# Performance work log

Hardware: AMD Instinct MI355X
Metric: run time of the kernel (lower is better)

## Reference

```python
import jax, jax.numpy as jnp
import numpy as np

B, S, HID = 2, 2048, 2048
NH, NKV, D = 32, 8, 64
M = 256          # FAVOR+ random features
CHUNK = 128      # causal chunk size
EPS = 1e-6


def setup_inputs():
    key = jax.random.key(0)
    ks = jax.random.split(key, 7)
    hidden_states = jax.random.normal(ks[0], (B, S, HID), jnp.float32)
    # RoPE tables (HF Llama style): [B, S, D]
    inv_freq = 1.0 / (10000.0 ** (jnp.arange(0, D, 2, dtype=jnp.float32) / D))
    freqs = jnp.arange(S, dtype=jnp.float32)[:, None] * inv_freq[None, :]   # [S, D/2]
    emb = jnp.concatenate([freqs, freqs], axis=-1)                          # [S, D]
    cos = jnp.broadcast_to(jnp.cos(emb)[None], (B, S, D)).astype(jnp.float32)
    sin = jnp.broadcast_to(jnp.sin(emb)[None], (B, S, D)).astype(jnp.float32)
    sc = 0.02
    Wq = jax.random.normal(ks[1], (NH * D, HID), jnp.float32) * sc
    Wk = jax.random.normal(ks[2], (NKV * D, HID), jnp.float32) * sc
    Wv = jax.random.normal(ks[3], (NKV * D, HID), jnp.float32) * sc
    Wo = jax.random.normal(ks[4], (HID, NH * D), jnp.float32) * sc
    proj = jax.random.normal(ks[5], (M, D), jnp.float32)  # FAVOR+ random projection
    return {"hidden_states": hidden_states, "cos": cos, "sin": sin,
            "Wq": Wq, "Wk": Wk, "Wv": Wv, "Wo": Wo, "proj": proj}


def rotate_half(x):
    x1, x2 = x[..., : x.shape[-1] // 2], x[..., x.shape[-1] // 2:]
    return jnp.concatenate([-x2, x1], axis=-1)


def favor_features(x, proj, is_query):
    # FAVOR+ positive softmax-kernel features: phi(x) = exp(Wx' - |x'|^2/2 - stab)/sqrt(m)
    dn = x.shape[-1] ** -0.25
    xn = x * dn                                            # data normalizer d^{-1/4}
    xp = jnp.einsum('bhsd,md->bhsm', xn, proj)             # [B,H,S,M]
    sq = 0.5 * jnp.sum(xn * xn, axis=-1, keepdims=True)
    if is_query:
        stab = jnp.max(xp, axis=-1, keepdims=True)
    else:
        stab = jnp.max(xp, axis=(-1, -2), keepdims=True)
    return (jnp.exp(xp - sq - stab) + EPS) / jnp.sqrt(jnp.asarray(M, xp.dtype))


def causal_linear_attention(phi_q, phi_k, v):
    # phi_q/phi_k: [B,H,S,M], v: [B,H,S,D]; causal chunked prefix formulation
    Bh, H, T, m = phi_q.shape
    d = v.shape[-1]
    nc = T // CHUNK
    qc = phi_q.reshape(Bh, H, nc, CHUNK, m)
    kc = phi_k.reshape(Bh, H, nc, CHUNK, m)
    vc = v.reshape(Bh, H, nc, CHUNK, d)
    # per-chunk KV state and key sums
    kv = jnp.einsum('bhscm,bhscd->bhsmd', kc, vc)          # [B,H,nc,M,D]
    kz = jnp.sum(kc, axis=3)                               # [B,H,nc,M]
    kv_pre = jnp.cumsum(kv, axis=2) - kv                   # exclusive prefix
    kz_pre = jnp.cumsum(kz, axis=2) - kz
    inter = jnp.einsum('bhscm,bhsmd->bhscd', qc, kv_pre)
    inter_z = jnp.einsum('bhscm,bhsm->bhsc', qc, kz_pre)
    # intra-chunk causal part
    mask = jnp.tril(jnp.ones((CHUNK, CHUNK), phi_q.dtype))
    scores = jnp.einsum('bhscm,bhstm->bhsct', qc, kc) * mask
    intra = jnp.einsum('bhsct,bhstd->bhscd', scores, vc)
    intra_z = jnp.sum(scores, axis=-1)
    out = (inter + intra) / (inter_z + intra_z + EPS)[..., None]
    return out.reshape(Bh, H, T, d)


def reference(hidden_states, cos, sin, Wq, Wk, Wv, Wo, proj):
    b, s, _ = hidden_states.shape
    q = (hidden_states @ Wq.T).reshape(b, s, NH, D).transpose(0, 2, 1, 3)   # [B,NH,S,D]
    k = (hidden_states @ Wk.T).reshape(b, s, NKV, D).transpose(0, 2, 1, 3)  # [B,NKV,S,D]
    v = (hidden_states @ Wv.T).reshape(b, s, NKV, D).transpose(0, 2, 1, 3)
    c, si = cos[:, None, :, :], sin[:, None, :, :]
    q = q * c + rotate_half(q) * si
    k = k * c + rotate_half(k) * si
    groups = NH // NKV
    k = jnp.repeat(k, groups, axis=1)
    v = jnp.repeat(v, groups, axis=1)
    phi_q = favor_features(q, proj, is_query=True)
    phi_k = favor_features(k, proj, is_query=False)
    attn = causal_linear_attention(phi_q, phi_k, v)                         # [B,NH,S,D]
    attn = attn.transpose(0, 2, 1, 3).reshape(b, s, NH * D)
    return attn @ Wo.T
```

## Files before the change

kernel.cpp:

```cpp
#include <hip/hip_runtime.h>
#include <hip/hip_bf16.h>

#define SEQ   2048
#define NHEAD 32
#define NKVH  8
#define DH    64
#define MFEAT 256
#define NCH   16
#define EPSF  1e-6f

typedef __hip_bfloat16 bf16;
typedef unsigned short u16;
typedef __attribute__((ext_vector_type(8))) short short8;
typedef __attribute__((ext_vector_type(4))) float f32x4;

__device__ __forceinline__ float b2f(bf16 x){ return __bfloat162float(x); }
__device__ __forceinline__ bf16  f2b(float x){ return __float2bfloat16(x); }
__device__ __forceinline__ u16   f2u(float x){ bf16 h = __float2bfloat16(x); return *reinterpret_cast<u16*>(&h); }

__device__ __forceinline__ bool probe_f32(const unsigned* __restrict__ p){
  return (p[0] & 0xFFFFu) == 0u;
}
__device__ __forceinline__ float loadIn(const void* __restrict__ ptr, size_t idx, bool f32){
  return f32 ? ((const float*)ptr)[idx] : b2f(((const bf16*)ptr)[idx]);
}

__device__ __forceinline__ void cp16(u16* lds, const u16* g){
  __builtin_amdgcn_global_load_lds((const __attribute__((address_space(1))) unsigned*)g,
      (__attribute__((address_space(3))) unsigned*)lds, 16, 0, 0);
}

#define MFMA16(a,b,c) __builtin_amdgcn_mfma_f32_16x16x32_bf16(a,b,c,0,0,0)

__global__ __launch_bounds__(256) void conv_kernel(const void* __restrict__ src,
    u16* __restrict__ dst, const unsigned* __restrict__ probe)
{
  const bool f32in = probe_f32(probe);
  size_t i = ((size_t)blockIdx.x*256 + threadIdx.x)*4;
  #pragma unroll
  for (int j=0;j<4;++j) dst[i+j] = f2u(loadIn(src, i+j, f32in));
}

__global__ __launch_bounds__(256) void gemm_mfma(const u16* __restrict__ A,
    const u16* __restrict__ W, float* __restrict__ oq, float* __restrict__ ok,
    float* __restrict__ ov, void* __restrict__ outAny, int K, int N, int mode,
    const void* __restrict__ cosg, const void* __restrict__ sing,
    const unsigned* __restrict__ probe)
{
  __shared__ __align__(16) u16 sA[4096];
  __shared__ __align__(16) u16 sB[4096];
  const int tid = threadIdx.x;
  const int lane = tid & 63, wave = tid >> 6;
  const int c0 = blockIdx.x*128, r0 = blockIdx.y*128;
  const int wm = wave & 1, wn = wave >> 1;
  f32x4 acc[4][4] = {};

  const int ch0 = wave*64 + lane, ch1 = 256 + wave*64 + lane;
  const u16* gA0 = A + (size_t)(r0 + (ch0>>2))*K + (ch0&3)*8;
  const u16* gA1 = A + (size_t)(r0 + (ch1>>2))*K + (ch1&3)*8;
  const u16* gB0 = W + (size_t)(c0 + (ch0>>2))*K + (ch0&3)*8;
  const u16* gB1 = W + (size_t)(c0 + (ch1>>2))*K + (ch1&3)*8;
  u16* lA0 = &sA[(wave*64)*8];  u16* lA1 = &sA[(256 + wave*64)*8];
  u16* lB0 = &sB[(wave*64)*8];  u16* lB1 = &sB[(256 + wave*64)*8];

  const u16* pA = &sA[(wm*64 + (lane&15))*32 + (lane>>4)*8];
  const u16* pB = &sB[(wn*64 + (lane&15))*32 + (lane>>4)*8];

  for (int k0 = 0; k0 < K; k0 += 32) {
    cp16(lA0, gA0 + k0); cp16(lA1, gA1 + k0);
    cp16(lB0, gB0 + k0); cp16(lB1, gB1 + k0);
    __syncthreads();
    short8 af[4], bfv[4];
    #pragma unroll
    for (int mt=0;mt<4;++mt) af[mt]  = *(const short8*)(pA + mt*512);
    #pragma unroll
    for (int nt=0;nt<4;++nt) bfv[nt] = *(const short8*)(pB + nt*512);
    #pragma unroll
    for (int mt=0;mt<4;++mt)
      #pragma unroll
      for (int nt=0;nt<4;++nt)
        acc[mt][nt] = MFMA16(af[mt], bfv[nt], acc[mt][nt]);
    __syncthreads();
  }

  const int rbase = r0 + wm*64 + (lane>>4)*4;
  const int cbase = c0 + wn*64 + (lane&15);
  if (mode == 0) {
    const bool f32o = probe_f32(probe);
    #pragma unroll
    for (int mt=0;mt<4;++mt)
      #pragma unroll
      for (int nt=0;nt<4;++nt)
        #pragma unroll
        for (int rg=0;rg<4;++rg){
          int r = rbase + mt*16 + rg, c = cbase + nt*16;
          float v = acc[mt][nt][rg];
          if (f32o) ((float*)outAny)[(size_t)r*N + c] = v;
          else      ((u16*)outAny)[(size_t)r*N + c] = f2u(v);
        }
  } else {
    const bool f32in = probe_f32(probe);
    const float dn = 0.3535533905932738f;
    #pragma unroll
    for (int nt=0;nt<4;++nt){
      int cc = cbase + nt*16;
      float* dst; int H2, cl; bool isv = false;
      if (cc < 2048){ dst = oq; H2 = 32; cl = cc; }
      else if (cc < 2560){ dst = ok; H2 = 8; cl = cc - 2048; }
      else { dst = ov; H2 = 8; cl = cc - 2560; isv = true; }
      int hh = cl>>6, dd = cl&63;
      float sgn = (dd < 32) ? -1.f : 1.f;
      #pragma unroll
      for (int mt=0;mt<4;++mt)
        #pragma unroll
        for (int rg=0;rg<4;++rg){
          int r = rbase + mt*16 + rg;
          int bb = r>>11, s = r&2047;
          float v = acc[mt][nt][rg];
          if (!isv){
            float vp = acc[mt][nt^2][rg];
            size_t ci = ((size_t)bb*SEQ + s)*DH + dd;
            float cv = loadIn(cosg, ci, f32in);
            float sv = loadIn(sing, ci, f32in);
            v = (v*cv + sgn*vp*sv) * dn;
          }
          dst[(((size_t)bb*H2 + hh)*SEQ + s)*DH + dd] = v;
        }
    }
  }
}

__global__ __launch_bounds__(256) void phi_mfma(const float* __restrict__ xn,
    const u16* __restrict__ projb, float* __restrict__ rmaxk,
    const float* __restrict__ stabk, u16* __restrict__ phi, int mode)
{
  __shared__ __align__(16) u16 sA[64*80];
  __shared__ __align__(16) u16 sP[256*80];
  __shared__ float sq[64];
  const int tid = threadIdx.x, lane = tid & 63, wave = tid >> 6;
  const size_t row0 = (size_t)blockIdx.x * 64;

  #pragma unroll
  for (int l = 0; l < 8; ++l){
    int v8 = tid + l*256;
    int off = v8*8; int m = off>>6, d = off&63;
    *(short8*)&sP[m*80 + d] = ((const short8*)projb)[v8];
  }
  {
    int r = tid >> 2, qq = tid & 3;
    const float* src = xn + (row0 + r)*DH + qq*16;
    float s = 0.f;
    u16 tmp[16];
    #pragma unroll
    for (int i=0;i<16;i+=4){
      float4 v4 = *(const float4*)&src[i];
      s += v4.x*v4.x + v4.y*v4.y + v4.z*v4.z + v4.w*v4.w;
      tmp[i] = f2u(v4.x); tmp[i+1] = f2u(v4.y); tmp[i+2] = f2u(v4.z); tmp[i+3] = f2u(v4.w);
    }
    *(short8*)&sA[r*80 + qq*16]     = *(short8*)&tmp[0];
    *(short8*)&sA[r*80 + qq*16 + 8] = *(short8*)&tmp[8];
    s += __shfl_xor(s, 1, 64);
    s += __shfl_xor(s, 2, 64);
    if (qq == 0) sq[r] = 0.5f*s;
  }
  __syncthreads();

  f32x4 acc[16] = {};
  const u16* pA = &sA[(wave*16 + (lane&15))*80 + (lane>>4)*8];
  short8 af0 = *(const short8*)(pA);
  short8 af1 = *(const short8*)(pA + 32);
  #pragma unroll
  for (int nt=0; nt<16; ++nt){
    const u16* pB = &sP[(nt*16 + (lane&15))*80 + (lane>>4)*8];
    short8 b0 = *(const short8*)(pB);
    short8 b1 = *(const short8*)(pB + 32);
    acc[nt] = MFMA16(af0, b0, acc[nt]);
    acc[nt] = MFMA16(af1, b1, acc[nt]);
  }

  float mx[4];
  #pragma unroll
  for (int rg=0; rg<4; ++rg){
    float m = acc[0][rg];
    #pragma unroll
    for (int nt=1; nt<16; ++nt) m = fmaxf(m, acc[nt][rg]);
    m = fmaxf(m, __shfl_xor(m, 1, 64));
    m = fmaxf(m, __shfl_xor(m, 2, 64));
    m = fmaxf(m, __shfl_xor(m, 4, 64));
    m = fmaxf(m, __shfl_xor(m, 8, 64));
    mx[rg] = m;
  }
  const int rloc = wave*16 + (lane>>4)*4;
  if (mode == 1){
    if ((lane & 15) == 0){
      #pragma unroll
      for (int rg=0;rg<4;++rg) rmaxk[row0 + rloc + rg] = mx[rg];
    }
    return;
  }
  float stab[4];
  if (mode == 0){
    #pragma unroll
    for (int rg=0;rg<4;++rg) stab[rg] = mx[rg];
  } else {
    float s = stabk[row0 >> 11];
    #pragma unroll
    for (int rg=0;rg<4;++rg) stab[rg] = s;
  }
  float sqr[4];
  #pragma unroll
  for (int rg=0;rg<4;++rg) sqr[rg] = sq[rloc + rg];
  #pragma unroll
  for (int nt=0;nt<16;++nt){
    #pragma unroll
    for (int rg=0;rg<4;++rg){
      float val = (__expf(fminf(acc[nt][rg] - sqr[rg] - stab[rg], 0.f)) + EPSF) * 0.0625f;
      phi[(row0 + rloc + rg)*MFEAT + nt*16 + (lane&15)] = f2u(val);
    }
  }
}

__global__ void stab_reduce_kernel(const float* __restrict__ rmaxk, float* __restrict__ stabk){
  __shared__ float red[256];
  int bk = blockIdx.x;
  float mx = -1e30f;
  for (int i = threadIdx.x; i < SEQ; i += 256) mx = fmaxf(mx, rmaxk[(size_t)bk*SEQ + i]);
  red[threadIdx.x] = mx; __syncthreads();
  for (int off=128; off>0; off>>=1){
    if ((int)threadIdx.x < off) red[threadIdx.x] = fmaxf(red[threadIdx.x], red[threadIdx.x+off]);
    __syncthreads();
  }
  if (threadIdx.x==0) stabk[bk] = red[0];
}

__global__ __launch_bounds__(256) void kvchunk_kernel(const bf16* __restrict__ phik,
    const float* __restrict__ vbuf, float* __restrict__ kv, float* __restrict__ kz)
{
  int blk = blockIdx.x; int bk = blk >> 4, c = blk & 15;
  const bf16* Kc = phik + ((size_t)bk*SEQ + c*128)*MFEAT;
  const float* Vc = vbuf + ((size_t)bk*SEQ + c*128)*DH;
  __shared__ float sV[128*64];
  for (int l=0;l<32;++l){ int idx = threadIdx.x + l*256; sV[idx] = Vc[idx]; }
  __syncthreads();
  int m = threadIdx.x;
  float acc[64] = {}; float az = 0.f;
  for (int t=0;t<128;++t){
    float ph = b2f(Kc[(size_t)t*MFEAT + m]);
    az += ph;
    const float4* vr = (const float4*)&sV[t*64];
    #pragma unroll
    for (int d4=0; d4<16; ++d4){
      float4 v4 = vr[d4];
      acc[d4*4+0] += ph*v4.x; acc[d4*4+1] += ph*v4.y;
      acc[d4*4+2] += ph*v4.z; acc[d4*4+3] += ph*v4.w;
    }
  }
  float* out = kv + (size_t)blk*MFEAT*DH + (size_t)m*DH;
  #pragma unroll
  for (int d4=0; d4<16; ++d4)
    ((float4*)out)[d4] = make_float4(acc[d4*4],acc[d4*4+1],acc[d4*4+2],acc[d4*4+3]);
  kz[(size_t)blk*MFEAT + m] = az;
}

__global__ void scan_kernel(float* __restrict__ p, int inner, int nc, int total){
  int t = blockIdx.x*256 + threadIdx.x;
  if (t >= total) return;
  int outer = t / inner, rem = t - outer*inner;
  float* base = p + (size_t)outer*nc*inner + rem;
  float run = 0.f;
  for (int c=0;c<nc;++c){
    float v = base[(size_t)c*inner];
    base[(size_t)c*inner] = run;
    run += v;
  }
}

__global__ __launch_bounds__(256) void attn_mfma(
    const u16* __restrict__ phiq, const u16* __restrict__ phik,
    const float* __restrict__ vbuf, const float* __restrict__ kvp,
    const float* __restrict__ kzp, u16* __restrict__ attnout)
{
  __shared__ __align__(16) u16 smem[28288];
  __shared__ float sZ[128];
  const int tid = threadIdx.x, lane = tid & 63, wave = tid >> 6;
  const int blk = blockIdx.x;
  const int c = blk & 15, h = (blk >> 4) & 31, b = blk >> 9;
  const int kvh = h >> 2;
  const u16* Q   = phiq + (((size_t)(b*NHEAD+h)*SEQ) + c*128)*MFEAT;
  const u16* Kc  = phik + (((size_t)(b*NKVH+kvh)*SEQ) + c*128)*MFEAT;
  const float* Vc  = vbuf + (((size_t)(b*NKVH+kvh)*SEQ) + c*128)*DH;
  const float* KVp = kvp + ((size_t)((b*NKVH+kvh)*NCH + c))*MFEAT*DH;
  const float* KZp = kzp + ((size_t)((b*NKVH+kvh)*NCH + c))*MFEAT;

  u16* sQ   = smem;
  u16* sK   = smem + 4096;
  u16* sKVT = smem + 8192;
  u16* sP   = smem;
  u16* sVT  = smem + 17408;

  f32x4 accS[2][8] = {};
  f32x4 accO[2][5] = {};

  const int ch0 = wave*64 + lane, ch1 = 256 + wave*64 + lane;
  const u16* gQ0 = Q  + (ch0>>2)*MFEAT + (ch0&3)*8;
  const u16* gQ1 = Q  + (ch1>>2)*MFEAT + (ch1&3)*8;
  const u16* gK0 = Kc + (ch0>>2)*MFEAT + (ch0&3)*8;
  const u16* gK1 = Kc + (ch1>>2)*MFEAT + (ch1&3)*8;
  u16* lQ0 = &sQ[(wave*64)*8];  u16* lQ1 = &sQ[(256+wave*64)*8];
  u16* lK0 = &sK[(wave*64)*8];  u16* lK1 = &sK[(256+wave*64)*8];

  for (int k0 = 0; k0 < MFEAT; k0 += 32) {
    cp16(lQ0, gQ0 + k0); cp16(lQ1, gQ1 + k0);
    cp16(lK0, gK0 + k0); cp16(lK1, gK1 + k0);
    #pragma unroll
    for (int i=0;i<8;++i){
      int idx = tid + i*256;
      int m = idx >> 6, d = idx & 63;
      sKVT[d*72 + m] = f2u(KVp[(size_t)(k0+m)*DH + d]);
    }
    if (tid < 32) sKVT[64*72 + tid] = f2u(KZp[k0 + tid]);
    __syncthreads();
    short8 af0, af1;
    const u16* pQ = &sQ[(wave*32 + (lane&15))*32 + (lane>>4)*8];
    af0 = *(const short8*)(pQ);
    af1 = *(const short8*)(pQ + 512);
    #pragma unroll
    for (int nt=0;nt<8;++nt){
      short8 bk = *(const short8*)&sK[(nt*16 + (lane&15))*32 + (lane>>4)*8];
      accS[0][nt] = MFMA16(af0, bk, accS[0][nt]);
      accS[1][nt] = MFMA16(af1, bk, accS[1][nt]);
    }
    #pragma unroll
    for (int nt=0;nt<5;++nt){
      short8 bi = *(const short8*)&sKVT[(nt*16 + (lane&15))*72 + (lane>>4)*8];
      accO[0][nt] = MFMA16(af0, bi, accO[0][nt]);
      accO[1][nt] = MFMA16(af1, bi, accO[1][nt]);
    }
    __syncthreads();
  }

  #pragma unroll
  for (int mt=0;mt<2;++mt){
    int rowb = wave*32 + mt*16 + (lane>>4)*4;
    #pragma unroll
    for (int nt=0;nt<8;++nt){
      int col = nt*16 + (lane&15);
      #pragma unroll
      for (int rg=0;rg<4;++rg){
        int row = rowb + rg;
        float v = (col <= row) ? accS[mt][nt][rg] : 0.f;
        sP[row*136 + col] = f2u(v);
      }
    }
  }
  #pragma unroll
  for (int i=0;i<32;++i){
    int idx = tid + i*256;
    int t = idx >> 6, d = idx & 63;
    sVT[d*136 + t] = f2u(Vc[idx]);
  }
  if (tid < 128) sVT[64*136 + tid] = 0x3F80;
  __syncthreads();

  #pragma unroll
  for (int kc=0;kc<4;++kc){
    const u16* pP = &sP[(wave*32 + (lane&15))*136 + kc*32 + (lane>>4)*8];
    short8 pa0 = *(const short8*)(pP);
    short8 pa1 = *(const short8*)(pP + 16*136);
    #pragma unroll
    for (int nt=0;nt<5;++nt){
      short8 bv = *(const short8*)&sVT[(nt*16 + (lane&15))*136 + kc*32 + (lane>>4)*8];
      accO[0][nt] = MFMA16(pa0, bv, accO[0][nt]);
      accO[1][nt] = MFMA16(pa1, bv, accO[1][nt]);
    }
  }

  if ((lane & 15) == 0){
    #pragma unroll
    for (int mt=0;mt<2;++mt){
      int rowb = wave*32 + mt*16 + (lane>>4)*4;
      #pragma unroll
      for (int rg=0;rg<4;++rg) sZ[rowb + rg] = accO[mt][4][rg];
    }
  }
  __syncthreads();
  const int d0 = lane & 15;
  #pragma unroll
  for (int mt=0;mt<2;++mt){
    int rowb = wave*32 + mt*16 + (lane>>4)*4;
    #pragma unroll
    for (int rg=0;rg<4;++rg){
      int row = rowb + rg;
      float inv = 1.0f / (sZ[row] + EPSF);
      int sg = c*128 + row;
      size_t ob = (((size_t)b*SEQ + sg)*NHEAD + h)*DH;
      #pragma unroll
      for (int nt=0;nt<4;++nt)
        attnout[ob + nt*16 + d0] = f2u(accO[mt][nt][rg] * inv);
    }
  }
}

extern "C" void kernel_launch(void* const* d_in, const int* in_sizes, int n_in,
                              void* d_out, int out_size, void* d_ws, size_t ws_size,
                              hipStream_t stream)
{
  const void* hidden = d_in[0];
  const void* cosg   = d_in[1];
  const void* sing   = d_in[2];
  const void* Wq     = d_in[3];
  const void* Wk     = d_in[4];
  const void* Wv     = d_in[5];
  const void* Wo     = d_in[6];
  const void* proj   = d_in[7];
  const unsigned* probe = (const unsigned*)d_in[1];

  float* ws = (float*)d_ws;
  float* xnq   = ws;
  float* kv    = ws;
  float* kz    = ws + 4194304;
  float* rmaxk = ws + 4259840;
  float* stabk = ws + 4292608;
  float* xnk   = ws + 8388608;
  float* vbuf  = ws + 10485760;
  u16*   projb = (u16*) (ws + 12582912);
  bf16*  phiq  = (bf16*)(ws + 12591104);
  bf16*  phik  = (bf16*)(ws + 29368320);
  u16*   hb    = (u16*) (ws + 33562624);
  u16*   attn  = (u16*) (ws + 33562624);
  u16*   wqkv  = (u16*) (ws + 37756928);
  u16*   wob   = (u16*) (ws + 37756928);

  conv_kernel<<<8192, 256, 0, stream>>>(hidden, hb, probe);
  conv_kernel<<<4096, 256, 0, stream>>>(Wq, wqkv,           probe);
  conv_kernel<<<1024, 256, 0, stream>>>(Wk, wqkv + 4194304, probe);
  conv_kernel<<<1024, 256, 0, stream>>>(Wv, wqkv + 5242880, probe);
  conv_kernel<<<16,   256, 0, stream>>>(proj, projb, probe);

  gemm_mfma<<<dim3(24,32), 256, 0, stream>>>(hb, wqkv, xnq, xnk, vbuf, nullptr,
                                             2048, 3072, 1, cosg, sing, probe);
  conv_kernel<<<4096, 256, 0, stream>>>(Wo, wob, probe);

  phi_mfma<<<2048, 256, 0, stream>>>(xnq, projb, nullptr, nullptr, (u16*)phiq, 0);
  phi_mfma<<<512,  256, 0, stream>>>(xnk, projb, rmaxk, nullptr, nullptr, 1);
  stab_reduce_kernel<<<16, 256, 0, stream>>>(rmaxk, stabk);
  phi_mfma<<<512,  256, 0, stream>>>(xnk, projb, nullptr, stabk, (u16*)phik, 2);

  kvchunk_kernel<<<256, 256, 0, stream>>>(phik, vbuf, kv, kz);
  scan_kernel<<<1024, 256, 0, stream>>>(kv, MFEAT*DH, NCH, 16*MFEAT*DH);
  scan_kernel<<<16,   256, 0, stream>>>(kz, MFEAT,    NCH, 16*MFEAT);

  attn_mfma<<<1024, 256, 0, stream>>>((const u16*)phiq, (const u16*)phik,
                                      vbuf, kv, kz, attn);

  gemm_mfma<<<dim3(16,32), 256, 0, stream>>>(attn, wob, nullptr, nullptr, nullptr,
                                             d_out, 2048, 2048, 0, nullptr, nullptr, probe);
}
```

Measured before the change: 498.5 us.

## Triple-buffer GEMM LDS tiles with async prefetch and swizzle workgroup order

The MFMA GEMM's K loop changes from a load-sync-compute-sync pattern to a three-stage LDS ring buffer. Tiles are prefetched two steps ahead, and vmcnt waits plus a single barrier per iteration replace the two __syncthreads. Workgroup IDs are also remapped in groups of 8 to improve L2 locality across blocks. This is meant to hide global-load latency behind MFMA work, at the cost of tripling LDS use, which may lower occupancy. It also depends on cp16 being an async direct-to-LDS load counted by vmcnt.

```diff
diff --git a/kernel.cpp b/kernel.cpp
--- a/kernel.cpp
+++ b/kernel.cpp
@@ -47,11 +47,19 @@
     const void* __restrict__ cosg, const void* __restrict__ sing,
     const unsigned* __restrict__ probe)
 {
-  __shared__ __align__(16) u16 sA[4096];
-  __shared__ __align__(16) u16 sB[4096];
+  __shared__ __align__(16) u16 sA[3][4096];
+  __shared__ __align__(16) u16 sB[3][4096];
   const int tid = threadIdx.x;
   const int lane = tid & 63, wave = tid >> 6;
-  const int c0 = blockIdx.x*128, r0 = blockIdx.y*128;
+
+  const int nbx = gridDim.x;
+  const int nwg = nbx * gridDim.y;
+  int id = blockIdx.y * nbx + blockIdx.x;
+  int sw = id;
+  if ((nwg & 7) == 0) sw = (id & 7) * (nwg >> 3) + (id >> 3);
+  const int bx = sw % nbx, by = sw / nbx;
+  const int c0 = bx*128, r0 = by*128;
+
   const int wm = wave & 1, wn = wave >> 1;
   f32x4 acc[4][4] = {};
 
@@ -60,16 +68,34 @@
   const u16* gA1 = A + (size_t)(r0 + (ch1>>2))*K + (ch1&3)*8;
   const u16* gB0 = W + (size_t)(c0 + (ch0>>2))*K + (ch0&3)*8;
   const u16* gB1 = W + (size_t)(c0 + (ch1>>2))*K + (ch1&3)*8;
-  u16* lA0 = &sA[(wave*64)*8];  u16* lA1 = &sA[(256 + wave*64)*8];
-  u16* lB0 = &sB[(wave*64)*8];  u16* lB1 = &sB[(256 + wave*64)*8];
-
-  const u16* pA = &sA[(wm*64 + (lane&15))*32 + (lane>>4)*8];
-  const u16* pB = &sB[(wn*64 + (lane&15))*32 + (lane>>4)*8];
-
-  for (int k0 = 0; k0 < K; k0 += 32) {
-    cp16(lA0, gA0 + k0); cp16(lA1, gA1 + k0);
-    cp16(lB0, gB0 + k0); cp16(lB1, gB1 + k0);
-    __syncthreads();
+  const int oA0 = (wave*64)*8, oA1 = (256 + wave*64)*8;
+
+  const int pAoff = (wm*64 + (lane&15))*32 + (lane>>4)*8;
+  const int pBoff = (wn*64 + (lane&15))*32 + (lane>>4)*8;
+
+  const int nk = K >> 5;
+
+  cp16(&sA[0][oA0], gA0);      cp16(&sA[0][oA1], gA1);
+  cp16(&sB[0][oA0], gB0);      cp16(&sB[0][oA1], gB1);
+  cp16(&sA[1][oA0], gA0 + 32); cp16(&sA[1][oA1], gA1 + 32);
+  cp16(&sB[1][oA0], gB0 + 32); cp16(&sB[1][oA1], gB1 + 32);
+
+  int cur = 0;
+  for (int t = 0; t < nk; ++t) {
+    if (t < nk-1) asm volatile("s_waitcnt vmcnt(4)" ::: "memory");
+    else          asm volatile("s_waitcnt vmcnt(0)" ::: "memory");
+    __builtin_amdgcn_s_barrier();
+    __builtin_amdgcn_sched_barrier(0);
+
+    if (t + 2 < nk) {
+      int stb = cur + 2; if (stb >= 3) stb -= 3;
+      const int k0 = (t + 2) * 32;
+      cp16(&sA[stb][oA0], gA0 + k0); cp16(&sA[stb][oA1], gA1 + k0);
+      cp16(&sB[stb][oA0], gB0 + k0); cp16(&sB[stb][oA1], gB1 + k0);
+    }
+
+    const u16* pA = &sA[cur][pAoff];
+    const u16* pB = &sB[cur][pBoff];
     short8 af[4], bfv[4];
     #pragma unroll
     for (int mt=0;mt<4;++mt) af[mt]  = *(const short8*)(pA + mt*512);
@@ -80,7 +106,8 @@
       #pragma unroll
       for (int nt=0;nt<4;++nt)
         acc[mt][nt] = MFMA16(af[mt], bfv[nt], acc[mt][nt]);
-    __syncthreads();
+
+    cur = (cur == 2) ? 0 : cur + 1;
   }
 
   const int rbase = r0 + wm*64 + (lane>>4)*4;
```

Measured after the change: 496.4 us. No clear change (-0.4%).

## Rewrite projection GEMMs as double-buffered 256x256 pipelined MFMA kernel with swizzled LDS

Applied to the files above, without the earlier changes.

Replaces the single-buffered 128x128 GEMM tile with a 512-thread 256x256 tile using BK=64, double-buffered LDS staged via global_load_lds interleaved with MFMA phases, XOR-swizzled LDS layout to avoid bank conflicts, block-id remapping across XCDs, and priority raising around MFMA bursts. The aim is to hide global load latency and raise data reuse in the QKV and output projections. It uses 128KB of LDS per block and far fewer blocks (192 and 128), which risks underfilling the 256 CUs and lowers occupancy.

```diff
diff --git a/kernel.cpp b/kernel.cpp
--- a/kernel.cpp
+++ b/kernel.cpp
@@ -31,6 +31,8 @@
 }
 
 #define MFMA16(a,b,c) __builtin_amdgcn_mfma_f32_16x16x32_bf16(a,b,c,0,0,0)
+#define SBAR()  do { __builtin_amdgcn_s_barrier(); __builtin_amdgcn_sched_barrier(0); } while(0)
+#define LGKM0() do { asm volatile("s_waitcnt lgkmcnt(0)" ::: "memory"); __builtin_amdgcn_sched_barrier(0); } while(0)
 
 __global__ __launch_bounds__(256) void conv_kernel(const void* __restrict__ src,
     u16* __restrict__ dst, const unsigned* __restrict__ probe)
@@ -41,54 +43,105 @@
   for (int j=0;j<4;++j) dst[i+j] = f2u(loadIn(src, i+j, f32in));
 }
 
-__global__ __launch_bounds__(256) void gemm_mfma(const u16* __restrict__ A,
+__global__ __launch_bounds__(512) void gemm_mfma(const u16* __restrict__ A,
     const u16* __restrict__ W, float* __restrict__ oq, float* __restrict__ ok,
     float* __restrict__ ov, void* __restrict__ outAny, int K, int N, int mode,
     const void* __restrict__ cosg, const void* __restrict__ sing,
     const unsigned* __restrict__ probe)
 {
-  __shared__ __align__(16) u16 sA[4096];
-  __shared__ __align__(16) u16 sB[4096];
+  __shared__ __align__(16) u16 sA[2][16384];
+  __shared__ __align__(16) u16 sB[2][16384];
   const int tid = threadIdx.x;
   const int lane = tid & 63, wave = tid >> 6;
-  const int c0 = blockIdx.x*128, r0 = blockIdx.y*128;
-  const int wm = wave & 1, wn = wave >> 1;
-  f32x4 acc[4][4] = {};
-
-  const int ch0 = wave*64 + lane, ch1 = 256 + wave*64 + lane;
-  const u16* gA0 = A + (size_t)(r0 + (ch0>>2))*K + (ch0&3)*8;
-  const u16* gA1 = A + (size_t)(r0 + (ch1>>2))*K + (ch1&3)*8;
-  const u16* gB0 = W + (size_t)(c0 + (ch0>>2))*K + (ch0&3)*8;
-  const u16* gB1 = W + (size_t)(c0 + (ch1>>2))*K + (ch1&3)*8;
-  u16* lA0 = &sA[(wave*64)*8];  u16* lA1 = &sA[(256 + wave*64)*8];
-  u16* lB0 = &sB[(wave*64)*8];  u16* lB1 = &sB[(256 + wave*64)*8];
-
-  const u16* pA = &sA[(wm*64 + (lane&15))*32 + (lane>>4)*8];
-  const u16* pB = &sB[(wn*64 + (lane&15))*32 + (lane>>4)*8];
-
-  for (int k0 = 0; k0 < K; k0 += 32) {
-    cp16(lA0, gA0 + k0); cp16(lA1, gA1 + k0);
-    cp16(lB0, gB0 + k0); cp16(lB1, gB1 + k0);
-    __syncthreads();
-    short8 af[4], bfv[4];
-    #pragma unroll
-    for (int mt=0;mt<4;++mt) af[mt]  = *(const short8*)(pA + mt*512);
-    #pragma unroll
-    for (int nt=0;nt<4;++nt) bfv[nt] = *(const short8*)(pB + nt*512);
-    #pragma unroll
-    for (int mt=0;mt<4;++mt)
-      #pragma unroll
-      for (int nt=0;nt<4;++nt)
-        acc[mt][nt] = MFMA16(af[mt], bfv[nt], acc[mt][nt]);
-    __syncthreads();
-  }
-
-  const int rbase = r0 + wm*64 + (lane>>4)*4;
+
+  const int nbx = gridDim.x;
+  const int nwg = nbx * gridDim.y;
+  int id = blockIdx.y * nbx + blockIdx.x;
+  int sw = id;
+  if ((nwg & 7) == 0) sw = (id & 7) * (nwg >> 3) + (id >> 3);
+  const int bx = sw % nbx, by = sw / nbx;
+  const int c0 = bx*256, r0 = by*256;
+
+  const int wm = wave >> 2, wn = wave & 3;
+  f32x4 acc[8][4] = {};
+
+  const int rl  = lane >> 3;
+  const int swzE = ((lane & 7) ^ rl) << 3;
+  const u16* gA = A + (size_t)(r0 + wave*16 + rl)*K + swzE;
+  const u16* gB = W + (size_t)(c0 + wave*16 + rl)*K + swzE;
+
+  const int rA0 = (wm*128 + (lane&15))*64;
+  const int rB0 = (wn*64  + (lane&15))*64;
+  const int colS = (((lane>>4)*8) ^ ((lane&7)<<3));
+
+  const int nk = K >> 6;
+
+  #define STAGE_A(tt, h) do { if ((tt) < nk){ const int b_=(tt)&1;          \
+      const int k0_=(tt)*64;                                                \
+      cp16(&sA[b_][(h)*8192 + wave*1024      ], gA + (size_t)((h)*128    )*K + k0_); \
+      cp16(&sA[b_][(h)*8192 + wave*1024 + 512], gA + (size_t)((h)*128 + 8)*K + k0_); } } while(0)
+  #define STAGE_B(tt, h) do { if ((tt) < nk){ const int b_=(tt)&1;          \
+      const int k0_=(tt)*64;                                                \
+      cp16(&sB[b_][(h)*8192 + wave*1024      ], gB + (size_t)((h)*128    )*K + k0_); \
+      cp16(&sB[b_][(h)*8192 + wave*1024 + 512], gB + (size_t)((h)*128 + 8)*K + k0_); } } while(0)
+
+  #define PHASE(q, ...) do {                                                \
+      aF[0][0] = *(const short8*)(bufA + rA0 + (2*(q)  )*1024 + colS);      \
+      aF[0][1] = *(const short8*)(bufA + rA0 + (2*(q)  )*1024 + (colS^32)); \
+      aF[1][0] = *(const short8*)(bufA + rA0 + (2*(q)+1)*1024 + colS);      \
+      aF[1][1] = *(const short8*)(bufA + rA0 + (2*(q)+1)*1024 + (colS^32)); \
+      __VA_ARGS__;                                                          \
+      SBAR();                                                               \
+      LGKM0();                                                              \
+      __builtin_amdgcn_s_setprio(1);                                        \
+      _Pragma("unroll")                                                     \
+      for (int i_=0;i_<2;++i_)                                              \
+        _Pragma("unroll")                                                   \
+        for (int nt_=0;nt_<4;++nt_){                                        \
+          acc[2*(q)+i_][nt_] = MFMA16(aF[i_][0], bF[nt_][0], acc[2*(q)+i_][nt_]); \
+          acc[2*(q)+i_][nt_] = MFMA16(aF[i_][1], bF[nt_][1], acc[2*(q)+i_][nt_]); \
+        }                                                                   \
+      __builtin_amdgcn_s_setprio(0);                                        \
+    } while(0)
+
+  STAGE_A(0,0); STAGE_A(0,1); STAGE_B(0,0); STAGE_B(0,1);
+  STAGE_B(1,0); STAGE_B(1,1);
+  asm volatile("s_waitcnt vmcnt(4)" ::: "memory");
+  SBAR();
+
+  for (int t = 0; t < nk; ++t) {
+    const u16* bufA = sA[t&1];
+    const u16* bufB = sB[t&1];
+    short8 bF[4][2], aF[2][2];
+
+    #pragma unroll
+    for (int nt=0;nt<4;++nt){
+      bF[nt][0] = *(const short8*)(bufB + rB0 + nt*1024 + colS);
+      bF[nt][1] = *(const short8*)(bufB + rB0 + nt*1024 + (colS^32));
+    }
+    PHASE(0, STAGE_A(t+1,0));
+    SBAR();
+    PHASE(1, STAGE_A(t+1,1));
+    SBAR();
+    PHASE(2, STAGE_B(t+2,0));
+    SBAR();
+    PHASE(3, STAGE_B(t+2,1));
+    if (t < nk-1){
+      if (t == nk-2) { asm volatile("s_waitcnt vmcnt(0)" ::: "memory"); }
+      else           { asm volatile("s_waitcnt vmcnt(4)" ::: "memory"); }
+      SBAR();
+    }
+  }
+  #undef PHASE
+  #undef STAGE_A
+  #undef STAGE_B
+
+  const int rbase = r0 + wm*128 + (lane>>4)*4;
   const int cbase = c0 + wn*64 + (lane&15);
   if (mode == 0) {
     const bool f32o = probe_f32(probe);
     #pragma unroll
-    for (int mt=0;mt<4;++mt)
+    for (int mt=0;mt<8;++mt)
       #pragma unroll
       for (int nt=0;nt<4;++nt)
         #pragma unroll
@@ -111,7 +164,7 @@
       int hh = cl>>6, dd = cl&63;
       float sgn = (dd < 32) ? -1.f : 1.f;
       #pragma unroll
-      for (int mt=0;mt<4;++mt)
+      for (int mt=0;mt<8;++mt)
         #pragma unroll
         for (int rg=0;rg<4;++rg){
           int r = rbase + mt*16 + rg;
@@ -437,7 +490,7 @@
   conv_kernel<<<1024, 256, 0, stream>>>(Wv, wqkv + 5242880, probe);
   conv_kernel<<<16,   256, 0, stream>>>(proj, projb, probe);
 
-  gemm_mfma<<<dim3(24,32), 256, 0, stream>>>(hb, wqkv, xnq, xnk, vbuf, nullptr,
+  gemm_mfma<<<dim3(12,16), 512, 0, stream>>>(hb, wqkv, xnq, xnk, vbuf, nullptr,
                                              2048, 3072, 1, cosg, sing, probe);
   conv_kernel<<<4096, 256, 0, stream>>>(Wo, wob, probe);
 
@@ -453,6 +506,6 @@
   attn_mfma<<<1024, 256, 0, stream>>>((const u16*)phiq, (const u16*)phik,
                                       vbuf, kv, kz, attn);
 
-  gemm_mfma<<<dim3(16,32), 256, 0, stream>>>(attn, wob, nullptr, nullptr, nullptr,
-                                             d_out, 2048, 2048, 0, nullptr, nullptr, probe);
-}
+  gemm_mfma<<<dim3(8,16), 512, 0, stream>>>(attn, wob, nullptr, nullptr, nullptr,
+                                            d_out, 2048, 2048, 0, nullptr, nullptr, probe);
+}
```

Result: faster. 488.5 us (-2.0%).
